# Performance work log

Measured on AMD Instinct MI355X. Metric: run time of the kernel, lower is better.

## Reference

```python
import jax, jax.numpy as jnp
import numpy as np

BBOX_POS_MAX = 1024.0
BN_EPS = 1e-5


def _bn_eval(x, g, b, rm, rv):
    # BatchNorm1d in eval mode: affine transform with running stats
    return g * (x - rm) * jax.lax.rsqrt(rv + BN_EPS) + b


def setup_inputs() -> dict:
    key = jax.random.key(0)
    ks = jax.random.split(key, 24)
    B, N, F = 32, 512, 1024
    E = 32768
    H1, H2, H3 = 512, 256, 128          # node_pred_hidden
    EH1, EH2 = 64, 64                   # edge_pred_hidden
    NC, EC = 8, 10                      # node/edge concept channels
    BC = 9                              # bbox_channels (4 bbox + 4 dir + 1 prio)
    s = 0.02
    inp = {
        'roi_features': jax.random.normal(ks[0], (B, N, F), jnp.float32),
        'batch_bboxes': jax.random.uniform(ks[1], (B, N, 4), jnp.float32) * BBOX_POS_MAX,
        'batch_directions': jax.random.uniform(ks[2], (B, N, 4), jnp.float32),
        'batch_priorities': jax.random.uniform(ks[3], (B, N), jnp.float32),
        'batch_edge_index': jax.random.randint(ks[4], (B, 2, E), 0, N, jnp.int32),
        # node_predictor params
        'np_w1': jax.random.normal(ks[5], (F, H1), jnp.float32) * s,
        'np_b1': jnp.zeros((H1,), jnp.float32),
        'bn1_g': jnp.ones((H1,), jnp.float32),
        'bn1_b': jnp.zeros((H1,), jnp.float32),
        'bn1_rm': jnp.zeros((H1,), jnp.float32),
        'bn1_rv': jnp.ones((H1,), jnp.float32),
        'np_w2': jax.random.normal(ks[6], (H1, H2), jnp.float32) * s,
        'np_b2': jnp.zeros((H2,), jnp.float32),
        'bn2_g': jnp.ones((H2,), jnp.float32),
        'bn2_b': jnp.zeros((H2,), jnp.float32),
        'bn2_rm': jnp.zeros((H2,), jnp.float32),
        'bn2_rv': jnp.ones((H2,), jnp.float32),
        'np_w3': jax.random.normal(ks[7], (H2, H3), jnp.float32) * s,
        'np_b3': jnp.zeros((H3,), jnp.float32),
        'ni_w': jax.random.normal(ks[8], (H3, NC), jnp.float32) * s,
        'ni_b': jnp.zeros((NC,), jnp.float32),
        # edge_predictor params (input dim = 2 * bbox_channels)
        'ep_w1': jax.random.normal(ks[9], (2 * BC, EH1), jnp.float32) * s,
        'ep_b1': jnp.zeros((EH1,), jnp.float32),
        'ep_w2': jax.random.normal(ks[10], (EH1, EH2), jnp.float32) * s,
        'ep_b2': jnp.zeros((EH2,), jnp.float32),
        'ei_w': jax.random.normal(ks[11], (EH2, EC), jnp.float32) * s,
        'ei_b': jnp.zeros((EC,), jnp.float32),
    }
    return inp


def reference(roi_features, batch_bboxes, batch_directions, batch_priorities,
              batch_edge_index,
              np_w1, np_b1, bn1_g, bn1_b, bn1_rm, bn1_rv,
              np_w2, np_b2, bn2_g, bn2_b, bn2_rm, bn2_rv,
              np_w3, np_b3, ni_w, ni_b,
              ep_w1, ep_b1, ep_w2, ep_b2, ei_w, ei_b):
    B, N, F = roi_features.shape
    # ---- node path: MLP (eval-mode BN, dropout = identity) + sigmoid interpreter
    x = roi_features.reshape(B * N, F)
    h = jax.nn.relu(_bn_eval(x @ np_w1 + np_b1, bn1_g, bn1_b, bn1_rm, bn1_rv))
    h = jax.nn.relu(_bn_eval(h @ np_w2 + np_b2, bn2_g, bn2_b, bn2_rm, bn2_rv))
    h = jax.nn.relu(h @ np_w3 + np_b3)
    node_concepts = jax.nn.sigmoid(h @ ni_w + ni_b).reshape(B, N, -1)
    # ---- edge path: per-batch gather of node attrs via edge_index, concat, MLP
    node_attr = jnp.concatenate(
        [batch_bboxes / BBOX_POS_MAX, batch_directions, batch_priorities[..., None]],
        axis=-1)  # [B, N, 9]
    C = node_attr.shape[-1]
    src_idx = batch_edge_index[:, 0, :, None]  # [B, E, 1]
    dst_idx = batch_edge_index[:, 1, :, None]
    src = jnp.take_along_axis(node_attr, src_idx.astype(jnp.int32), axis=1)  # [B, E, 9]
    dst = jnp.take_along_axis(node_attr, dst_idx.astype(jnp.int32), axis=1)
    edge_attr = jnp.concatenate([src, dst], axis=-1).reshape(-1, 2 * C)  # [B*E, 18]
    e = jax.nn.relu(edge_attr @ ep_w1 + ep_b1)
    e = jax.nn.relu(e @ ep_w2 + ep_b2)
    edge_concepts = jax.nn.sigmoid(e @ ei_w + ei_b)  # [B*E, EC]
    return node_concepts, edge_concepts
```

## Files before the change

kernel.cpp:

```cpp
#include <hip/hip_runtime.h>
#include <cstdint>
#include <cstddef>

#define BN_EPSF 1e-5f

constexpr int B_  = 32, N_ = 512, F_ = 1024, E_ = 32768;
constexpr int H1_ = 512, H2_ = 256, H3_ = 128, NC_ = 8, EC_ = 10;
constexpr int M_  = B_ * N_;
constexpr int NE_ = B_ * E_;

typedef short bf16x8 __attribute__((ext_vector_type(8)));
typedef float f32x4  __attribute__((ext_vector_type(4)));

__device__ __forceinline__ short f2bf(float f) {
  union { float f; unsigned u; } v; v.f = f;
  unsigned r = v.u + 0x7fffu + ((v.u >> 16) & 1u);
  return (short)(r >> 16);
}
__device__ __forceinline__ unsigned cvtpk(float a, float b) {
  unsigned r;
  asm("v_cvt_pk_bf16_f32 %0, %1, %2" : "=v"(r) : "v"(a), "v"(b));
  return r;
}

#define GLDS(gp, lp) __builtin_amdgcn_global_load_lds( \
    (const __attribute__((address_space(1))) void*)(gp), \
    (__attribute__((address_space(3))) void*)(lp), 16, 0, 0)

#define MFMA(a, b, c) __builtin_amdgcn_mfma_f32_16x16x32_bf16((a), (b), (c), 0, 0, 0)

__device__ __forceinline__ void wt_body(
    const float* __restrict__ W, short* __restrict__ Wt, int K, int N,
    int bx, int by, float (*s)[33])
{
  const int tx = threadIdx.x & 31, ty = threadIdx.x >> 5;
  const int k0 = by * 32, n0 = bx * 32;
#pragma unroll
  for (int r = 0; r < 4; r++)
    s[ty * 4 + r][tx] = W[(size_t)(k0 + ty * 4 + r) * N + n0 + tx];
  __syncthreads();
#pragma unroll
  for (int r = 0; r < 4; r++)
    Wt[(size_t)(n0 + ty * 4 + r) * K + k0 + tx] = f2bf(s[tx][ty * 4 + r]);
}

__global__ __launch_bounds__(256) void k_prep(
    const float* __restrict__ roi, ushort* __restrict__ roiB,
    const float* __restrict__ w1, short* __restrict__ w1t,
    const float* __restrict__ w2, short* __restrict__ w2t,
    const float* __restrict__ w3, short* __restrict__ w3t)
{
  __shared__ float s[32][33];
  const int bx = blockIdx.x;
  if (bx < 8192) {
    int i = bx * 256 + threadIdx.x;
    float4 a = *(const float4*)(roi + (size_t)i * 8);
    float4 b = *(const float4*)(roi + (size_t)i * 8 + 4);
    unsigned o[4];
    o[0] = cvtpk(a.x, a.y); o[1] = cvtpk(a.z, a.w);
    o[2] = cvtpk(b.x, b.y); o[3] = cvtpk(b.z, b.w);
    *(uint4*)(roiB + (size_t)i * 8) = *(uint4*)o;
  } else if (bx < 8704) {
    int idx = bx - 8192; wt_body(w1, w1t, F_, H1_, idx & 15, idx >> 4, s);
  } else if (bx < 8832) {
    int idx = bx - 8704; wt_body(w2, w2t, H1_, H2_, idx & 7, idx >> 3, s);
  } else {
    int idx = bx - 8832; wt_body(w3, w3t, H2_, H3_, idx & 3, idx >> 2, s);
  }
}

__device__ __forceinline__ void relu_pack_shuf(
    const f32x4 (&acc)[4], int la, int lb, bool lo32, bf16x8 (&out)[2])
{
  unsigned plo[4], phi[4];
#pragma unroll
  for (int t = 0; t < 4; t++) {
    plo[t] = cvtpk(fmaxf(acc[t][0], 0.f), fmaxf(acc[t][1], 0.f));
    phi[t] = cvtpk(fmaxf(acc[t][2], 0.f), fmaxf(acc[t][3], 0.f));
  }
#pragma unroll
  for (int ks = 0; ks < 2; ks++) {
    unsigned w0a = (unsigned)__shfl((int)plo[2 * ks], la);
    unsigned w0b = (unsigned)__shfl((int)plo[2 * ks + 1], la);
    unsigned w1a = (unsigned)__shfl((int)phi[2 * ks], la);
    unsigned w1b = (unsigned)__shfl((int)phi[2 * ks + 1], la);
    unsigned w2a = (unsigned)__shfl((int)plo[2 * ks], lb);
    unsigned w2b = (unsigned)__shfl((int)plo[2 * ks + 1], lb);
    unsigned w3a = (unsigned)__shfl((int)phi[2 * ks], lb);
    unsigned w3b = (unsigned)__shfl((int)phi[2 * ks + 1], lb);
    union { unsigned u[4]; bf16x8 v; } t;
    t.u[0] = lo32 ? w0a : w0b;
    t.u[1] = lo32 ? w1a : w1b;
    t.u[2] = lo32 ? w2a : w2b;
    t.u[3] = lo32 ? w3a : w3b;
    out[ks] = t.v;
  }
}

__global__ __launch_bounds__(256, 3) void k_fused(
    const float* __restrict__ bbox, const float* __restrict__ dir,
    const float* __restrict__ pri, const int* __restrict__ eidx,
    const float* __restrict__ ew1, const float* __restrict__ eb1,
    const float* __restrict__ ew2, const float* __restrict__ eb2,
    const float* __restrict__ eow, const float* __restrict__ eob,
    float* __restrict__ out_edge,
    const short* __restrict__ roiB, const short* __restrict__ w1t,
    const float* __restrict__ b1, const float* __restrict__ g1,
    const float* __restrict__ bb1, const float* __restrict__ rm1,
    const float* __restrict__ rv1, short* __restrict__ h1)
{
  __shared__ __align__(16) char arena[30720];

  const int bx = blockIdx.x;
  const int rsel = bx % 3;
  const int tid  = threadIdx.x;
  const int wave = tid >> 6, lane = tid & 63;
  const int lm = lane & 15;

  if (rsel == 2) {
    const int lb = bx / 3;
    short* As = (short*)arena;
    short* Bs = (short*)(arena + 8192);
    const int m0 = (lb >> 2) * 128, n0 = (lb & 3) * 128;
    const int wm = wave >> 1, wn = wave & 1;
    const int arow = tid >> 2;
    const int akq  = (tid & 3) * 8;

    f32x4 acc[4][4] = {};
    for (int k0 = 0; k0 < F_; k0 += 32) {
#pragma unroll
      for (int it = 0; it < 2; it++)
        GLDS(roiB + (size_t)(m0 + it * 64 + arow) * F_ + k0 + akq,
             (char*)As + it * 4096 + wave * 1024);
#pragma unroll
      for (int it = 0; it < 2; it++)
        GLDS(w1t + (size_t)(n0 + it * 64 + arow) * F_ + k0 + akq,
             (char*)Bs + it * 4096 + wave * 1024);
      __syncthreads();

      const int ko = (lane >> 4) * 8;
      bf16x8 af[4], bfr[4];
#pragma unroll
      for (int t = 0; t < 4; t++) {
        af[t]  = *(const bf16x8*)&As[(wm * 64 + t * 16 + lm) * 32 + ko];
        bfr[t] = *(const bf16x8*)&Bs[(wn * 64 + t * 16 + lm) * 32 + ko];
      }
#pragma unroll
      for (int ti = 0; ti < 4; ti++)
#pragma unroll
        for (int tj = 0; tj < 4; tj++)
          acc[ti][tj] = MFMA(af[ti], bfr[tj], acc[ti][tj]);
      __syncthreads();
    }
#pragma unroll
    for (int tj = 0; tj < 4; tj++) {
      const int col = n0 + wn * 64 + tj * 16 + lm;
      const float bi = b1[col];
      float s = g1[col] * rsqrtf(rv1[col] + BN_EPSF);
      float t = bb1[col] - rm1[col] * s;
#pragma unroll
      for (int ti = 0; ti < 4; ti++) {
        const int rbase = m0 + wm * 64 + ti * 16 + ((lane >> 4) << 2);
#pragma unroll
        for (int r = 0; r < 4; r += 2) {
          float va = fmaf(acc[ti][tj][r]     + bi, s, t);
          float vb = fmaf(acc[ti][tj][r + 1] + bi, s, t);
          unsigned p = cvtpk(fmaxf(va, 0.f), fmaxf(vb, 0.f));
          h1[(size_t)(rbase + r)     * H1_ + col] = (short)p;
          h1[(size_t)(rbase + r + 1) * H1_ + col] = (short)(p >> 16);
        }
      }
    }
    return;
  }

  const int eb    = (bx / 3) * 2 + rsel;
  const int batch = eb >> 5;
  const int q     = lane >> 4;

  short*  sW1   = (short*)arena;
  short*  sW2   = (short*)(arena + 4096);
  short*  sW3   = (short*)(arena + 12288);
  ushort* sAttr = (ushort*)(arena + 14336);

  for (int i = tid; i < 2048; i += 256) {
    int n = i >> 5, k = i & 31;
    short v = 0;
    if (k < 9)                  v = f2bf(ew1[k * 64 + n]);
    else if (k >= 16 && k < 25) v = f2bf(ew1[(k - 7) * 64 + n]);
    sW1[i] = v;
  }
  for (int i = tid; i < 4096; i += 256) {
    int n = i >> 6, k = i & 63;
    sW2[i] = f2bf(ew2[k * 64 + n]);
  }
  for (int i = tid; i < 1024; i += 256) {
    int n = i >> 6, k = i & 63;
    sW3[i] = (n < 10) ? f2bf(eow[k * 10 + n]) : (short)0;
  }
  {
    const float inv = 1.0f / 1024.0f;
    for (int n = tid; n < 512; n += 256) {
      int gi = batch * 512 + n;
      float4 bv = *(const float4*)(bbox + (size_t)gi * 4);
      float4 dv = *(const float4*)(dir + (size_t)gi * 4);
      float pp = pri[gi];
      uint4 lo, hi;
      lo.x = cvtpk(bv.x * inv, bv.y * inv); lo.y = cvtpk(bv.z * inv, bv.w * inv);
      lo.z = cvtpk(dv.x, dv.y);             lo.w = cvtpk(dv.z, dv.w);
      hi.x = cvtpk(pp, 0.f); hi.y = 0; hi.z = 0; hi.w = 0;
      *(uint4*)&sAttr[n * 16]     = lo;
      *(uint4*)&sAttr[n * 16 + 8] = hi;
    }
  }
  __syncthreads();

  f32x4 b1q[4], b2q[4], boq;
#pragma unroll
  for (int t = 0; t < 4; t++) {
    b1q[t] = *(const f32x4*)(eb1 + t * 16 + q * 4);
    b2q[t] = *(const f32x4*)(eb2 + t * 16 + q * 4);
  }
#pragma unroll
  for (int r = 0; r < 4; r++)
    boq[r] = (q * 4 + r < 10) ? eob[q * 4 + r] : 0.f;

  const int  la   = (lane & 15) | ((lane & 16) << 1);
  const int  lbn  = la + 16;
  const bool lo32 = (lane < 32);
  const int* ip   = eidx + (size_t)batch * 2 * E_ + ((lane >= 32) ? E_ : 0);
  const int  ebl  = (eb & 31) * 1024;
  const int  ah   = (lane & 16) ? 16 : 0;

  for (int bi = 0; bi < 8; bi++) {
    const int kb = ebl + bi * 128 + wave * 32 + lm;

    bf16x8 xf[2];
#pragma unroll
    for (int ti = 0; ti < 2; ti++) {
      int kk   = (kb + ti * 16) & (E_ - 1);
      int node = ip[kk];
      xf[ti] = *(const bf16x8*)&sAttr[node * 16 + ah];
    }

    f32x4 acc1[2][4];
#pragma unroll
    for (int tj = 0; tj < 4; tj++) {
      bf16x8 fw1 = *(const bf16x8*)&sW1[(tj * 16 + lm) * 32 + q * 8];
#pragma unroll
      for (int ti = 0; ti < 2; ti++)
        acc1[ti][tj] = MFMA(fw1, xf[ti], b1q[tj]);
    }
    bf16x8 xf2[2][2];
#pragma unroll
    for (int ti = 0; ti < 2; ti++)
      relu_pack_shuf(acc1[ti], la, lbn, lo32, xf2[ti]);

    f32x4 acc2[2][4];
#pragma unroll
    for (int ti = 0; ti < 2; ti++)
#pragma unroll
      for (int tj = 0; tj < 4; tj++)
        acc2[ti][tj] = b2q[tj];
#pragma unroll
    for (int ks = 0; ks < 2; ks++)
#pragma unroll
      for (int tj = 0; tj < 4; tj++) {
        bf16x8 fw2 = *(const bf16x8*)&sW2[(tj * 16 + lm) * 64 + ks * 32 + q * 8];
#pragma unroll
        for (int ti = 0; ti < 2; ti++)
          acc2[ti][tj] = MFMA(fw2, xf2[ti][ks], acc2[ti][tj]);
      }
    bf16x8 xf3[2][2];
#pragma unroll
    for (int ti = 0; ti < 2; ti++)
      relu_pack_shuf(acc2[ti], la, lbn, lo32, xf3[ti]);

    bf16x8 fw3[2];
#pragma unroll
    for (int ks = 0; ks < 2; ks++)
      fw3[ks] = *(const bf16x8*)&sW3[lm * 64 + ks * 32 + q * 8];
#pragma unroll
    for (int ti = 0; ti < 2; ti++) {
      f32x4 a3 = boq;
#pragma unroll
      for (int ks = 0; ks < 2; ks++)
        a3 = MFMA(fw3[ks], xf3[ti][ks], a3);
      float o[4];
#pragma unroll
      for (int r = 0; r < 4; r++)
        o[r] = 1.f / (1.f + __expf(-a3[r]));
      size_t base = (size_t)(eb * 1024 + bi * 128 + wave * 32 + ti * 16 + lm) * 10;
      if (q == 0) {
        float2 t0; t0.x = o[0]; t0.y = o[1]; *(float2*)(out_edge + base)     = t0;
        float2 t1; t1.x = o[2]; t1.y = o[3]; *(float2*)(out_edge + base + 2) = t1;
      } else if (q == 1) {
        float2 t0; t0.x = o[0]; t0.y = o[1]; *(float2*)(out_edge + base + 4) = t0;
        float2 t1; t1.x = o[2]; t1.y = o[3]; *(float2*)(out_edge + base + 6) = t1;
      } else if (q == 2) {
        float2 t0; t0.x = o[0]; t0.y = o[1]; *(float2*)(out_edge + base + 8) = t0;
      }
    }
  }
}

__global__ __launch_bounds__(256) void k_tail(
    const short* __restrict__ h1, const short* __restrict__ w2t,
    const short* __restrict__ w3t,
    const float* __restrict__ b2, const float* __restrict__ g2,
    const float* __restrict__ bb2, const float* __restrict__ rm2,
    const float* __restrict__ rv2,
    const float* __restrict__ b3, const float* __restrict__ niw,
    const float* __restrict__ nib, float* __restrict__ out)
{
  __shared__ __align__(16) char arena[53760];
  short* sA  = (short*)arena;
  short* sB  = (short*)(arena + 4096);
  short* sH2 = (short*)(arena + 36864);
  short* sB3 = (short*)arena;
  short* sH3 = (short*)(arena + 16384);

  const int tid  = threadIdx.x;
  const int wave = tid >> 6, lane = tid & 63;
  const int lm = lane & 15, q = lane >> 4;
  const int wm = wave >> 1, wn = wave & 1;
  const int m0 = blockIdx.x * 32;
  const int srow = tid >> 2;
  const int skq  = (tid & 3) * 8;

  f32x4 acc2[8] = {};
  for (int k0 = 0; k0 < 512; k0 += 64) {
    {
      int c = tid >> 7, row = (tid >> 2) & 31;
      GLDS(h1 + (size_t)(m0 + row) * 512 + k0 + c * 32 + skq,
           (char*)sA + wave * 1024);
    }
#pragma unroll
    for (int it = 0; it < 4; it++)
#pragma unroll
      for (int c = 0; c < 2; c++)
        GLDS(w2t + (size_t)(it * 64 + srow) * 512 + k0 + c * 32 + skq,
             (char*)sB + c * 16384 + it * 4096 + wave * 1024);
    __syncthreads();
#pragma unroll
    for (int c = 0; c < 2; c++) {
      bf16x8 af = *(const bf16x8*)&sA[c * 1024 + (wm * 16 + lm) * 32 + q * 8];
#pragma unroll
      for (int nt = 0; nt < 8; nt++) {
        bf16x8 bfr = *(const bf16x8*)&sB[c * 8192 + (wn * 128 + nt * 16 + lm) * 32 + q * 8];
        acc2[nt] = MFMA(af, bfr, acc2[nt]);
      }
    }
    __syncthreads();
  }
#pragma unroll
  for (int nt = 0; nt < 8; nt++) {
    int col = wn * 128 + nt * 16 + lm;
    float s = g2[col] * rsqrtf(rv2[col] + BN_EPSF);
    float t = bb2[col] - rm2[col] * s;
    float bi = b2[col];
    float v0 = fmaf(acc2[nt][0] + bi, s, t);
    float v1 = fmaf(acc2[nt][1] + bi, s, t);
    float v2 = fmaf(acc2[nt][2] + bi, s, t);
    float v3 = fmaf(acc2[nt][3] + bi, s, t);
    unsigned p01 = cvtpk(fmaxf(v0, 0.f), fmaxf(v1, 0.f));
    unsigned p23 = cvtpk(fmaxf(v2, 0.f), fmaxf(v3, 0.f));
    int rb = wm * 16 + q * 4;
    sH2[(rb + 0) * 264 + col] = (short)p01;
    sH2[(rb + 1) * 264 + col] = (short)(p01 >> 16);
    sH2[(rb + 2) * 264 + col] = (short)p23;
    sH2[(rb + 3) * 264 + col] = (short)(p23 >> 16);
  }
  __syncthreads();

  f32x4 acc3[4] = {};
  for (int k0 = 0; k0 < 256; k0 += 64) {
#pragma unroll
    for (int it = 0; it < 2; it++)
#pragma unroll
      for (int c = 0; c < 2; c++)
        GLDS(w3t + (size_t)(it * 64 + srow) * 256 + k0 + c * 32 + skq,
             (char*)sB3 + c * 8192 + it * 4096 + wave * 1024);
    __syncthreads();
#pragma unroll
    for (int c = 0; c < 2; c++) {
      bf16x8 af = *(const bf16x8*)&sH2[(wm * 16 + lm) * 264 + k0 + c * 32 + q * 8];
#pragma unroll
      for (int nt = 0; nt < 4; nt++) {
        bf16x8 bfr = *(const bf16x8*)&sB3[c * 4096 + (wn * 64 + nt * 16 + lm) * 32 + q * 8];
        acc3[nt] = MFMA(af, bfr, acc3[nt]);
      }
    }
    __syncthreads();
  }
#pragma unroll
  for (int nt = 0; nt < 4; nt++) {
    int col = wn * 64 + nt * 16 + lm;
    float bi = b3[col];
    float v0 = acc3[nt][0] + bi;
    float v1 = acc3[nt][1] + bi;
    float v2 = acc3[nt][2] + bi;
    float v3 = acc3[nt][3] + bi;
    unsigned p01 = cvtpk(fmaxf(v0, 0.f), fmaxf(v1, 0.f));
    unsigned p23 = cvtpk(fmaxf(v2, 0.f), fmaxf(v3, 0.f));
    int rb = wm * 16 + q * 4;
    sH3[(rb + 0) * 136 + col] = (short)p01;
    sH3[(rb + 1) * 136 + col] = (short)(p01 >> 16);
    sH3[(rb + 2) * 136 + col] = (short)p23;
    sH3[(rb + 3) * 136 + col] = (short)(p23 >> 16);
  }
  __syncthreads();

  if (wave < 2) {
    f32x4 a4 = {};
#pragma unroll
    for (int c = 0; c < 4; c++) {
      ushort tmp[8];
#pragma unroll
      for (int j = 0; j < 8; j++) {
        int k = c * 32 + q * 8 + j;
        tmp[j] = (lm < 8) ? (ushort)f2bf(niw[k * 8 + lm]) : (ushort)0;
      }
      bf16x8 fw = *(bf16x8*)tmp;
      bf16x8 af4 = *(const bf16x8*)&sH3[(wave * 16 + lm) * 136 + c * 32 + q * 8];
      a4 = MFMA(af4, fw, a4);
    }
    if (lm < 8) {
      float bi = nib[lm];
#pragma unroll
      for (int r = 0; r < 4; r++) {
        float v = a4[r] + bi;
        out[(size_t)(m0 + wave * 16 + q * 4 + r) * 8 + lm] = 1.f / (1.f + __expf(-v));
      }
    }
  }
}

extern "C" void kernel_launch(void* const* d_in, const int* in_sizes, int n_in,
                              void* d_out, int out_size, void* d_ws, size_t ws_size,
                              hipStream_t stream)
{
  const float* roi   = (const float*)d_in[0];
  const float* bbox  = (const float*)d_in[1];
  const float* dir   = (const float*)d_in[2];
  const float* pri   = (const float*)d_in[3];
  const int*   eidx  = (const int*)d_in[4];
  const float* w1    = (const float*)d_in[5];
  const float* b1    = (const float*)d_in[6];
  const float* g1    = (const float*)d_in[7];
  const float* bb1   = (const float*)d_in[8];
  const float* rm1   = (const float*)d_in[9];
  const float* rv1   = (const float*)d_in[10];
  const float* w2    = (const float*)d_in[11];
  const float* b2    = (const float*)d_in[12];
  const float* g2    = (const float*)d_in[13];
  const float* bb2   = (const float*)d_in[14];
  const float* rm2   = (const float*)d_in[15];
  const float* rv2   = (const float*)d_in[16];
  const float* w3    = (const float*)d_in[17];
  const float* b3    = (const float*)d_in[18];
  const float* niw   = (const float*)d_in[19];
  const float* nib   = (const float*)d_in[20];
  const float* ew1   = (const float*)d_in[21];
  const float* eb1   = (const float*)d_in[22];
  const float* ew2   = (const float*)d_in[23];
  const float* eb2   = (const float*)d_in[24];
  const float* eow   = (const float*)d_in[25];
  const float* eob   = (const float*)d_in[26];

  float* out_node = (float*)d_out;
  float* out_edge = (float*)d_out + (size_t)M_ * NC_;

  char* w = (char*)d_ws;
  short*  roiB = (short*)w;
  short*  w1t  = (short*)(w + 33554432);
  short*  w2t  = (short*)(w + 34603008);
  short*  w3t  = (short*)(w + 34865152);
  short*  h1   = (short*)(w + 35717120);

  k_prep<<<8864, 256, 0, stream>>>(roi, (ushort*)roiB, w1, w1t, w2, w2t,
                                   w3, w3t);

  k_fused<<<1536, 256, 0, stream>>>(
      bbox, dir, pri, eidx, ew1, eb1, ew2, eb2, eow, eob, out_edge,
      roiB, w1t, b1, g1, bb1, rm1, rv1, h1);

  k_tail<<<M_ / 32, 256, 0, stream>>>(
      h1, w2t, w3t, b2, g2, bb2, rm2, rv2, b3, niw, nib, out_node);
}
```

Baseline: 255.1 us.

## Fuse ROI bf16 conversion into layer-1 GEMM and pipeline edge gathers

The standalone pass that converted roi_features to bf16 in workspace is removed. The layer-1 GEMM now loads fp32 rows directly, packs them to bf16 in registers and writes them to LDS, which saves a full write and re-read of the converted matrix. The cost is synchronous fp32 loads, twice the bytes per tile, in place of async global-to-LDS copies. The edge MLP now keeps its weight fragments in registers, prefetches all edge indices, and double-buffers the node-attribute gather across iterations. It also changes the attribute half offset from 16 to 8, which fixes which part of the node's attributes is read.

```diff
diff --git a/kernel.cpp b/kernel.cpp
--- a/kernel.cpp
+++ b/kernel.cpp
@@ -45,27 +45,18 @@
 }
 
 __global__ __launch_bounds__(256) void k_prep(
-    const float* __restrict__ roi, ushort* __restrict__ roiB,
     const float* __restrict__ w1, short* __restrict__ w1t,
     const float* __restrict__ w2, short* __restrict__ w2t,
     const float* __restrict__ w3, short* __restrict__ w3t)
 {
   __shared__ float s[32][33];
   const int bx = blockIdx.x;
-  if (bx < 8192) {
-    int i = bx * 256 + threadIdx.x;
-    float4 a = *(const float4*)(roi + (size_t)i * 8);
-    float4 b = *(const float4*)(roi + (size_t)i * 8 + 4);
-    unsigned o[4];
-    o[0] = cvtpk(a.x, a.y); o[1] = cvtpk(a.z, a.w);
-    o[2] = cvtpk(b.x, b.y); o[3] = cvtpk(b.z, b.w);
-    *(uint4*)(roiB + (size_t)i * 8) = *(uint4*)o;
-  } else if (bx < 8704) {
-    int idx = bx - 8192; wt_body(w1, w1t, F_, H1_, idx & 15, idx >> 4, s);
-  } else if (bx < 8832) {
-    int idx = bx - 8704; wt_body(w2, w2t, H1_, H2_, idx & 7, idx >> 3, s);
+  if (bx < 512) {
+    wt_body(w1, w1t, F_, H1_, bx & 15, bx >> 4, s);
+  } else if (bx < 640) {
+    int idx = bx - 512; wt_body(w2, w2t, H1_, H2_, idx & 7, idx >> 3, s);
   } else {
-    int idx = bx - 8832; wt_body(w3, w3t, H2_, H3_, idx & 3, idx >> 2, s);
+    int idx = bx - 640; wt_body(w3, w3t, H2_, H3_, idx & 3, idx >> 2, s);
   }
 }
 
@@ -104,7 +95,7 @@
     const float* __restrict__ ew2, const float* __restrict__ eb2,
     const float* __restrict__ eow, const float* __restrict__ eob,
     float* __restrict__ out_edge,
-    const short* __restrict__ roiB, const short* __restrict__ w1t,
+    const float* __restrict__ roi, const short* __restrict__ w1t,
     const float* __restrict__ b1, const float* __restrict__ g1,
     const float* __restrict__ bb1, const float* __restrict__ rm1,
     const float* __restrict__ rv1, short* __restrict__ h1)
@@ -125,17 +116,25 @@
     const int wm = wave >> 1, wn = wave & 1;
     const int arow = tid >> 2;
     const int akq  = (tid & 3) * 8;
+    const int r2   = tid >> 1;
+    const int h16  = (tid & 1) * 16;
+    const float* aprow = roi + (size_t)(m0 + r2) * F_ + h16;
 
     f32x4 acc[4][4] = {};
     for (int k0 = 0; k0 < F_; k0 += 32) {
-#pragma unroll
-      for (int it = 0; it < 2; it++)
-        GLDS(roiB + (size_t)(m0 + it * 64 + arow) * F_ + k0 + akq,
-             (char*)As + it * 4096 + wave * 1024);
+      const float4* ap = (const float4*)(aprow + k0);
+      float4 a0 = ap[0], a1 = ap[1], a2 = ap[2], a3 = ap[3];
 #pragma unroll
       for (int it = 0; it < 2; it++)
         GLDS(w1t + (size_t)(n0 + it * 64 + arow) * F_ + k0 + akq,
              (char*)Bs + it * 4096 + wave * 1024);
+      uint4 p0, p1;
+      p0.x = cvtpk(a0.x, a0.y); p0.y = cvtpk(a0.z, a0.w);
+      p0.z = cvtpk(a1.x, a1.y); p0.w = cvtpk(a1.z, a1.w);
+      p1.x = cvtpk(a2.x, a2.y); p1.y = cvtpk(a2.z, a2.w);
+      p1.z = cvtpk(a3.x, a3.y); p1.w = cvtpk(a3.z, a3.w);
+      *(uint4*)&As[r2 * 32 + h16]     = p0;
+      *(uint4*)&As[r2 * 32 + h16 + 8] = p1;
       __syncthreads();
 
       const int ko = (lane >> 4) * 8;
@@ -215,6 +214,19 @@
   }
   __syncthreads();
 
+  bf16x8 fW1[4], fW2[4][2], fW3[2];
+#pragma unroll
+  for (int t = 0; t < 4; t++)
+    fW1[t] = *(const bf16x8*)&sW1[(t * 16 + lm) * 32 + q * 8];
+#pragma unroll
+  for (int t = 0; t < 4; t++)
+#pragma unroll
+    for (int ks = 0; ks < 2; ks++)
+      fW2[t][ks] = *(const bf16x8*)&sW2[(t * 16 + lm) * 64 + ks * 32 + q * 8];
+#pragma unroll
+  for (int ks = 0; ks < 2; ks++)
+    fW3[ks] = *(const bf16x8*)&sW3[lm * 64 + ks * 32 + q * 8];
+
   f32x4 b1q[4], b2q[4], boq;
 #pragma unroll
   for (int t = 0; t < 4; t++) {
@@ -230,27 +242,35 @@
   const bool lo32 = (lane < 32);
   const int* ip   = eidx + (size_t)batch * 2 * E_ + ((lane >= 32) ? E_ : 0);
   const int  ebl  = (eb & 31) * 1024;
-  const int  ah   = (lane & 16) ? 16 : 0;
-
+  const int  ah   = (lane & 16) ? 8 : 0;
+
+  int nidx[8][2];
+#pragma unroll
+  for (int b = 0; b < 8; b++)
+#pragma unroll
+    for (int ti = 0; ti < 2; ti++)
+      nidx[b][ti] = ip[ebl + b * 128 + wave * 32 + ti * 16 + lm];
+
+  bf16x8 xf[2];
+#pragma unroll
+  for (int ti = 0; ti < 2; ti++)
+    xf[ti] = *(const bf16x8*)&sAttr[nidx[0][ti] * 16 + ah];
+
+#pragma unroll
   for (int bi = 0; bi < 8; bi++) {
-    const int kb = ebl + bi * 128 + wave * 32 + lm;
-
-    bf16x8 xf[2];
-#pragma unroll
-    for (int ti = 0; ti < 2; ti++) {
-      int kk   = (kb + ti * 16) & (E_ - 1);
-      int node = ip[kk];
-      xf[ti] = *(const bf16x8*)&sAttr[node * 16 + ah];
+    bf16x8 xn[2];
+    if (bi < 7) {
+#pragma unroll
+      for (int ti = 0; ti < 2; ti++)
+        xn[ti] = *(const bf16x8*)&sAttr[nidx[bi + 1][ti] * 16 + ah];
     }
 
     f32x4 acc1[2][4];
 #pragma unroll
-    for (int tj = 0; tj < 4; tj++) {
-      bf16x8 fw1 = *(const bf16x8*)&sW1[(tj * 16 + lm) * 32 + q * 8];
+    for (int tj = 0; tj < 4; tj++)
 #pragma unroll
       for (int ti = 0; ti < 2; ti++)
-        acc1[ti][tj] = MFMA(fw1, xf[ti], b1q[tj]);
-    }
+        acc1[ti][tj] = MFMA(fW1[tj], xf[ti], b1q[tj]);
     bf16x8 xf2[2][2];
 #pragma unroll
     for (int ti = 0; ti < 2; ti++)
@@ -265,27 +285,21 @@
 #pragma unroll
     for (int ks = 0; ks < 2; ks++)
 #pragma unroll
-      for (int tj = 0; tj < 4; tj++) {
-        bf16x8 fw2 = *(const bf16x8*)&sW2[(tj * 16 + lm) * 64 + ks * 32 + q * 8];
+      for (int tj = 0; tj < 4; tj++)
 #pragma unroll
         for (int ti = 0; ti < 2; ti++)
-          acc2[ti][tj] = MFMA(fw2, xf2[ti][ks], acc2[ti][tj]);
-      }
+          acc2[ti][tj] = MFMA(fW2[tj][ks], xf2[ti][ks], acc2[ti][tj]);
     bf16x8 xf3[2][2];
 #pragma unroll
     for (int ti = 0; ti < 2; ti++)
       relu_pack_shuf(acc2[ti], la, lbn, lo32, xf3[ti]);
 
-    bf16x8 fw3[2];
-#pragma unroll
-    for (int ks = 0; ks < 2; ks++)
-      fw3[ks] = *(const bf16x8*)&sW3[lm * 64 + ks * 32 + q * 8];
 #pragma unroll
     for (int ti = 0; ti < 2; ti++) {
       f32x4 a3 = boq;
 #pragma unroll
       for (int ks = 0; ks < 2; ks++)
-        a3 = MFMA(fw3[ks], xf3[ti][ks], a3);
+        a3 = MFMA(fW3[ks], xf3[ti][ks], a3);
       float o[4];
 #pragma unroll
       for (int r = 0; r < 4; r++)
@@ -301,6 +315,7 @@
         float2 t0; t0.x = o[0]; t0.y = o[1]; *(float2*)(out_edge + base + 8) = t0;
       }
     }
+    xf[0] = xn[0]; xf[1] = xn[1];
   }
 }
 
@@ -472,18 +487,16 @@
   float* out_edge = (float*)d_out + (size_t)M_ * NC_;
 
   char* w = (char*)d_ws;
-  short*  roiB = (short*)w;
-  short*  w1t  = (short*)(w + 33554432);
-  short*  w2t  = (short*)(w + 34603008);
-  short*  w3t  = (short*)(w + 34865152);
-  short*  h1   = (short*)(w + 35717120);
-
-  k_prep<<<8864, 256, 0, stream>>>(roi, (ushort*)roiB, w1, w1t, w2, w2t,
-                                   w3, w3t);
+  short*  w1t  = (short*)w;
+  short*  w2t  = (short*)(w + 1048576);
+  short*  w3t  = (short*)(w + 1310720);
+  short*  h1   = (short*)(w + 1376256);
+
+  k_prep<<<672, 256, 0, stream>>>(w1, w1t, w2, w2t, w3, w3t);
 
   k_fused<<<1536, 256, 0, stream>>>(
       bbox, dir, pri, eidx, ew1, eb1, ew2, eb2, eow, eob, out_edge,
-      roiB, w1t, b1, g1, bb1, rm1, rv1, h1);
+      roi, w1t, b1, g1, bb1, rm1, rv1, h1);
 
   k_tail<<<M_ / 32, 256, 0, stream>>>(
       h1, w2t, w3t, b2, g2, bb2, rm2, rv2, b3, niw, nib, out_node);
```

Measured after the change: 262.1 us. 2.7% more time.
